# Kernel tuning notes

Measured on AMD Instinct MI355X. Metric: run time of the kernel, lower is better.

## Reference

```python
import jax, jax.numpy as jnp
import numpy as np

N, H, W = 4096, 96, 96
C0 = 0.28209479177387814
C1 = 0.4886025119029199
C2 = [1.0925484305920792, -1.0925484305920792, 0.31539156525252005, -1.0925484305920792, 0.5462742152960396]
C3 = [-0.5900435899266435, 2.890611442640554, -0.4570457994644658, 0.3731763325901154, -0.4570457994644658, 1.445305721320277, -0.5900435899266435]


def setup_inputs() -> dict:
    key = jax.random.key(0)
    ks = jax.random.split(key, 6)
    return {
        'pws': jax.random.normal(ks[0], (N, 3), jnp.float32),
        'low_shs': 0.5 * jax.random.normal(ks[1], (N, 3), jnp.float32),
        'high_shs': 0.1 * jax.random.normal(ks[2], (N, 45), jnp.float32),
        'alphas_raw': jax.random.normal(ks[3], (N, 1), jnp.float32),
        'scales_raw': 0.5 * jax.random.normal(ks[4], (N, 3), jnp.float32) - 3.0,
        'rots_raw': jax.random.normal(ks[5], (N, 4), jnp.float32),
        'us': jnp.zeros((N, 2), jnp.float32),
        'Rcw': jnp.eye(3, dtype=jnp.float32),
        'tcw': jnp.array([0.0, 0.0, 4.0], jnp.float32),
        'cam_intr': jnp.array([120.0, 120.0, 48.0, 48.0], jnp.float32),  # fx fy cx cy
    }


def quat_to_rot(q):
    w, x, y, z = q[:, 0], q[:, 1], q[:, 2], q[:, 3]
    return jnp.stack([
        jnp.stack([1 - 2 * (y * y + z * z), 2 * (x * y - w * z), 2 * (x * z + w * y)], -1),
        jnp.stack([2 * (x * y + w * z), 1 - 2 * (x * x + z * z), 2 * (y * z - w * x)], -1),
        jnp.stack([2 * (x * z - w * y), 2 * (y * z + w * x), 1 - 2 * (x * x + y * y)], -1),
    ], -2)  # [N,3,3]


def sh2color(shs, dirs):
    # shs [N,16,3], dirs [N,3] normalized view directions
    x, y, z = dirs[:, 0:1], dirs[:, 1:2], dirs[:, 2:3]
    xx, yy, zz = x * x, y * y, z * z
    xy, yz, xz = x * y, y * z, x * z
    c = C0 * shs[:, 0]
    c = c - C1 * y * shs[:, 1] + C1 * z * shs[:, 2] - C1 * x * shs[:, 3]
    c = (c + C2[0] * xy * shs[:, 4] + C2[1] * yz * shs[:, 5]
         + C2[2] * (2 * zz - xx - yy) * shs[:, 6]
         + C2[3] * xz * shs[:, 7] + C2[4] * (xx - yy) * shs[:, 8])
    c = (c + C3[0] * y * (3 * xx - yy) * shs[:, 9] + C3[1] * xy * z * shs[:, 10]
         + C3[2] * y * (4 * zz - xx - yy) * shs[:, 11]
         + C3[3] * z * (2 * zz - 3 * xx - 3 * yy) * shs[:, 12]
         + C3[4] * x * (4 * zz - xx - yy) * shs[:, 13]
         + C3[5] * z * (xx - yy) * shs[:, 14]
         + C3[6] * x * (xx - 3 * yy) * shs[:, 15])
    return jnp.maximum(c + 0.5, 0.0)  # [N,3]


def _forward(pws, low_shs, high_shs, alphas_raw, scales_raw, rots_raw, Rcw, tcw, cam_intr):
    fx, fy, cx, cy = cam_intr[0], cam_intr[1], cam_intr[2], cam_intr[3]
    alphas = jax.nn.sigmoid(alphas_raw)[:, 0]                 # get_alphas
    scales = jnp.exp(scales_raw)                              # get_scales
    rots = rots_raw / jnp.linalg.norm(rots_raw, axis=1, keepdims=True)  # get_rots
    shs = jnp.concatenate([low_shs, high_shs], axis=1).reshape(-1, 16, 3)

    # --- project ---
    pcs = pws @ Rcw.T + tcw                                   # [N,3] camera coords
    depths = pcs[:, 2]
    zs = jnp.where(depths > 1e-6, depths, 1e-6)
    u = jnp.stack([fx * pcs[:, 0] / zs + cx, fy * pcs[:, 1] / zs + cy], axis=1)

    # --- cov3d = (R S)(R S)^T ---
    M = quat_to_rot(rots) * scales[:, None, :]
    cov3d = M @ jnp.swapaxes(M, 1, 2)                          # [N,3,3]

    # --- cov2d = J W cov3d W^T J^T + 0.3 I ---
    limx, limy = 1.3 * (W / (2.0 * fx)), 1.3 * (H / (2.0 * fy))
    tx = jnp.clip(pcs[:, 0] / zs, -limx, limx) * zs
    ty = jnp.clip(pcs[:, 1] / zs, -limy, limy) * zs
    zero = jnp.zeros_like(zs)
    J = jnp.stack([
        jnp.stack([fx / zs, zero, -fx * tx / (zs * zs)], -1),
        jnp.stack([zero, fy / zs, -fy * ty / (zs * zs)], -1),
    ], -2)                                                     # [N,2,3]
    T = J @ Rcw
    cov2d = T @ cov3d @ jnp.swapaxes(T, 1, 2)
    a = cov2d[:, 0, 0] + 0.3
    b = cov2d[:, 0, 1]
    c2 = cov2d[:, 1, 1] + 0.3

    # --- inverseCov2D + areas (radius of 3-sigma ellipse) ---
    det = a * c2 - b * b
    cinv = jnp.stack([c2, -b, a], axis=1) / det[:, None]       # [N,3]
    mid = 0.5 * (a + c2)
    lam = mid + jnp.sqrt(jnp.maximum(mid * mid - det, 0.1))
    radius = jnp.ceil(3.0 * jnp.sqrt(lam))
    areas = jnp.stack([radius, radius], axis=1)                # [N,2]

    # --- sh2Color ---
    twc = -(Rcw.T @ tcw)
    dirs = pws - twc
    dirs = dirs / jnp.linalg.norm(dirs, axis=1, keepdims=True)
    colors = sh2color(shs, dirs)                               # [N,3]

    # --- splat: depth-sorted alpha compositing ---
    valid = depths > 0.2
    order = jnp.argsort(depths)
    u_s, cinv_s = u[order], cinv[order]
    alpha_s, color_s, valid_s = alphas[order], colors[order], valid[order]

    px = (jnp.arange(W, dtype=jnp.float32))[None, :].repeat(H, 0).reshape(-1)
    py = (jnp.arange(H, dtype=jnp.float32))[:, None].repeat(W, 1).reshape(-1)
    dx = u_s[:, 0:1] - px[None, :]                             # [N,P]
    dy = u_s[:, 1:2] - py[None, :]
    power = -0.5 * (cinv_s[:, 0:1] * dx * dx + cinv_s[:, 2:3] * dy * dy) - cinv_s[:, 1:2] * dx * dy
    ap = jnp.minimum(alpha_s[:, None] * jnp.exp(jnp.minimum(power, 0.0)), 0.99)
    ap = jnp.where((ap >= 1.0 / 255.0) & valid_s[:, None], ap, 0.0)
    logt = jnp.cumsum(jnp.log1p(-ap), axis=0)
    tau = jnp.exp(jnp.concatenate([jnp.zeros((1, ap.shape[1])), logt[:-1]], axis=0))
    wgt = jnp.where(tau > 1e-4, ap * tau, 0.0)                 # [N,P]
    image = jnp.einsum('nc,np->cp', color_s, wgt).reshape(3, H, W)
    return image, areas


def reference(pws, low_shs, high_shs, alphas_raw, scales_raw, rots_raw, us, Rcw, tcw, cam_intr):
    return _forward(pws, low_shs, high_shs, alphas_raw, scales_raw, rots_raw, Rcw, tcw, cam_intr)
```

## Files before the change

kernel.cpp:

```cpp
#include <hip/hip_runtime.h>
#include <hip/hip_bf16.h>
#include <math.h>

#define GS_N 4096
#define IMG_H 96
#define IMG_W 96
#define NPIX (IMG_H * IMG_W)
#define TILE_PX 12
#define TILES_X 8
#define NTILES (TILES_X * TILES_X)
#define WAVES_PER_TILE 36

#define SH_C0 0.28209479177387814f
#define SH_C1 0.4886025119029199f
__device__ __constant__ float kC2[5] = {1.0925484305920792f, -1.0925484305920792f, 0.31539156525252005f, -1.0925484305920792f, 0.5462742152960396f};
__device__ __constant__ float kC3[7] = {-0.5900435899266435f, 2.890611442640554f, -0.4570457994644658f, 0.3731763325901154f, -0.4570457994644658f, 1.445305721320277f, -0.5900435899266435f};

__global__ __launch_bounds__(256) void gs_prep(
    const float* __restrict__ pws, const float* __restrict__ low_shs,
    const float* __restrict__ high_shs, const float* __restrict__ alphas_raw,
    const float* __restrict__ scales_raw, const float* __restrict__ rots_raw,
    const float* __restrict__ Rcw, const float* __restrict__ tcw,
    const float* __restrict__ cam,
    float* __restrict__ areas_out,
    float* __restrict__ depth_ws,
    int*   __restrict__ rank_ws,
    float4* __restrict__ A_uns,
    float4* __restrict__ B_uns,
    float* __restrict__ C_uns,
    float4* __restrict__ D_uns)
{
    int i = blockIdx.x * 256 + threadIdx.x;
    if (i >= GS_N) return;

    rank_ws[i] = 0;

    float fx = cam[0], fy = cam[1], cxi = cam[2], cyi = cam[3];
    float R0 = Rcw[0], R1 = Rcw[1], R2 = Rcw[2];
    float R3 = Rcw[3], R4 = Rcw[4], R5 = Rcw[5];
    float R6 = Rcw[6], R7 = Rcw[7], R8 = Rcw[8];
    float t0 = tcw[0], t1 = tcw[1], t2 = tcw[2];

    float pwx = pws[3*i+0], pwy = pws[3*i+1], pwz = pws[3*i+2];

    float pcx = R0*pwx + R1*pwy + R2*pwz + t0;
    float pcy = R3*pwx + R4*pwy + R5*pwz + t1;
    float pcz = R6*pwx + R7*pwy + R8*pwz + t2;

    float depth = pcz;
    float zs = (depth > 1e-6f) ? depth : 1e-6f;

    float ux = fx * pcx / zs + cxi;
    float uy = fy * pcy / zs + cyi;

    float alpha = 1.0f / (1.0f + expf(-alphas_raw[i]));

    float s0 = expf(scales_raw[3*i+0]);
    float s1 = expf(scales_raw[3*i+1]);
    float s2 = expf(scales_raw[3*i+2]);

    float qw = rots_raw[4*i+0], qx = rots_raw[4*i+1], qy = rots_raw[4*i+2], qz = rots_raw[4*i+3];
    float qn = sqrtf(qw*qw + qx*qx + qy*qy + qz*qz);
    qw /= qn; qx /= qn; qy /= qn; qz /= qn;

    float r00 = 1.0f - 2.0f*(qy*qy + qz*qz);
    float r01 = 2.0f*(qx*qy - qw*qz);
    float r02 = 2.0f*(qx*qz + qw*qy);
    float r10 = 2.0f*(qx*qy + qw*qz);
    float r11 = 1.0f - 2.0f*(qx*qx + qz*qz);
    float r12 = 2.0f*(qy*qz - qw*qx);
    float r20 = 2.0f*(qx*qz - qw*qy);
    float r21 = 2.0f*(qy*qz + qw*qx);
    float r22 = 1.0f - 2.0f*(qx*qx + qy*qy);

    float m00 = r00*s0, m01 = r01*s1, m02 = r02*s2;
    float m10 = r10*s0, m11 = r11*s1, m12 = r12*s2;
    float m20 = r20*s0, m21 = r21*s1, m22 = r22*s2;

    float V00 = m00*m00 + m01*m01 + m02*m02;
    float V01 = m00*m10 + m01*m11 + m02*m12;
    float V02 = m00*m20 + m01*m21 + m02*m22;
    float V11 = m10*m10 + m11*m11 + m12*m12;
    float V12 = m10*m20 + m11*m21 + m12*m22;
    float V22 = m20*m20 + m21*m21 + m22*m22;

    float limx = 1.3f * ((float)IMG_W / (2.0f * fx));
    float limy = 1.3f * ((float)IMG_H / (2.0f * fy));
    float xzr = pcx / zs, yzr = pcy / zs;
    float txv = fminf(fmaxf(xzr, -limx), limx) * zs;
    float tyv = fminf(fmaxf(yzr, -limy), limy) * zs;

    float J00 = fx / zs, J02 = -fx * txv / (zs * zs);
    float J11 = fy / zs, J12 = -fy * tyv / (zs * zs);

    float T00 = J00*R0 + J02*R6, T01 = J00*R1 + J02*R7, T02 = J00*R2 + J02*R8;
    float T10 = J11*R3 + J12*R6, T11 = J11*R4 + J12*R7, T12 = J11*R5 + J12*R8;

    float TW00 = T00*V00 + T01*V01 + T02*V02;
    float TW01 = T00*V01 + T01*V11 + T02*V12;
    float TW02 = T00*V02 + T01*V12 + T02*V22;
    float TW10 = T10*V00 + T11*V01 + T12*V02;
    float TW11 = T10*V01 + T11*V11 + T12*V12;
    float TW12 = T10*V02 + T11*V12 + T12*V22;

    float c00 = TW00*T00 + TW01*T01 + TW02*T02;
    float c01 = TW00*T10 + TW01*T11 + TW02*T12;
    float c11 = TW10*T10 + TW11*T11 + TW12*T12;

    float a  = c00 + 0.3f;
    float b  = c01;
    float cc = c11 + 0.3f;
    float det = a * cc - b * b;
    float ci0 = cc / det;
    float ci1 = -b / det;
    float ci2 = a / det;

    float mid = 0.5f * (a + cc);
    float lam = mid + sqrtf(fmaxf(mid * mid - det, 0.1f));
    float radius = ceilf(3.0f * sqrtf(lam));
    areas_out[2*i + 0] = radius;
    areas_out[2*i + 1] = radius;

    float twcx = -(R0*t0 + R3*t1 + R6*t2);
    float twcy = -(R1*t0 + R4*t1 + R7*t2);
    float twcz = -(R2*t0 + R5*t1 + R8*t2);
    float dx = pwx - twcx, dy = pwy - twcy, dz = pwz - twcz;
    float dn = sqrtf(dx*dx + dy*dy + dz*dz);
    dx /= dn; dy /= dn; dz /= dn;

    float xx = dx*dx, yy = dy*dy, zz = dz*dz;
    float xy = dx*dy, yz = dy*dz, xz = dx*dz;

    float bas0  = SH_C0;
    float bas1  = -SH_C1 * dy;
    float bas2  =  SH_C1 * dz;
    float bas3  = -SH_C1 * dx;
    float bas4  = kC2[0] * xy;
    float bas5  = kC2[1] * yz;
    float bas6  = kC2[2] * (2.0f*zz - xx - yy);
    float bas7  = kC2[3] * xz;
    float bas8  = kC2[4] * (xx - yy);
    float bas9  = kC3[0] * dy * (3.0f*xx - yy);
    float bas10 = kC3[1] * xy * dz;
    float bas11 = kC3[2] * dy * (4.0f*zz - xx - yy);
    float bas12 = kC3[3] * dz * (2.0f*zz - 3.0f*xx - 3.0f*yy);
    float bas13 = kC3[4] * dx * (4.0f*zz - xx - yy);
    float bas14 = kC3[5] * dz * (xx - yy);
    float bas15 = kC3[6] * dx * (xx - 3.0f*yy);

    float col[3];
    #pragma unroll
    for (int c = 0; c < 3; ++c) {
        const float* hs = high_shs + 45*i + c;
        float acc = bas0 * low_shs[3*i + c];
        acc += bas1  * hs[0*3];
        acc += bas2  * hs[1*3];
        acc += bas3  * hs[2*3];
        acc += bas4  * hs[3*3];
        acc += bas5  * hs[4*3];
        acc += bas6  * hs[5*3];
        acc += bas7  * hs[6*3];
        acc += bas8  * hs[7*3];
        acc += bas9  * hs[8*3];
        acc += bas10 * hs[9*3];
        acc += bas11 * hs[10*3];
        acc += bas12 * hs[11*3];
        acc += bas13 * hs[12*3];
        acc += bas14 * hs[13*3];
        acc += bas15 * hs[14*3];
        col[c] = fmaxf(acc + 0.5f, 0.0f);
    }

    bool valid = depth > 0.2f;
    float al_eff = valid ? alpha : 0.0f;

    float Tthr = __logf(255.0f * al_eff) + 1e-4f;
    float rx = (Tthr > 0.0f) ? sqrtf(2.0f * Tthr * a)  : -1.0f;
    float ry = (Tthr > 0.0f) ? sqrtf(2.0f * Tthr * cc) : -1.0f;

    depth_ws[i] = depth;
    A_uns[i] = make_float4(ux, uy, ci0, ci1);
    B_uns[i] = make_float4(ci2, al_eff, col[0], col[1]);
    C_uns[i] = col[2];
    D_uns[i] = make_float4(ux, uy, rx, ry);
}

__global__ __launch_bounds__(256) void gs_rank_partial(
    const float* __restrict__ depth, int* __restrict__ rank_ws)
{
    __shared__ float sd[256];
    int itile = blockIdx.x >> 4;
    int jtile = blockIdx.x & 15;
    int tid = threadIdx.x;
    int i = itile * 256 + tid;

    sd[tid] = depth[jtile * 256 + tid];
    __syncthreads();

    float mg = depth[i];
    int jbase = jtile * 256;
    int rank = 0;
    const float4* s4 = (const float4*)sd;
    #pragma unroll 16
    for (int jj = 0; jj < 64; ++jj) {
        float4 v = s4[jj];
        int j0 = jbase + jj * 4;
        rank += (v.x < mg || (v.x == mg && (j0+0) < i)) ? 1 : 0;
        rank += (v.y < mg || (v.y == mg && (j0+1) < i)) ? 1 : 0;
        rank += (v.z < mg || (v.z == mg && (j0+2) < i)) ? 1 : 0;
        rank += (v.w < mg || (v.w == mg && (j0+3) < i)) ? 1 : 0;
    }
    atomicAdd(&rank_ws[i], rank);
}

__global__ __launch_bounds__(256) void gs_gather(
    const int* __restrict__ rank_ws,
    const float4* __restrict__ A_uns, const float4* __restrict__ B_uns,
    const float* __restrict__ C_uns, const float4* __restrict__ D_uns,
    float4* __restrict__ A_s, float4* __restrict__ B_s, float* __restrict__ C_s,
    float4* __restrict__ D_s)
{
    int i = blockIdx.x * 256 + threadIdx.x;
    int r = rank_ws[i];
    A_s[r] = A_uns[i];
    B_s[r] = B_uns[i];
    C_s[r] = C_uns[i];
    D_s[r] = D_uns[i];
}

__global__ __launch_bounds__(256) void gs_bin(
    const float4* __restrict__ D_s,
    int* __restrict__ tile_list, int* __restrict__ tile_cnt)
{
    __shared__ int s_base;
    __shared__ int warp_off[4];
    int tile = blockIdx.x;
    int tx = tile & (TILES_X - 1), ty = tile >> 3;
    float x0 = (float)(tx * TILE_PX), x1 = (float)(tx * TILE_PX + TILE_PX - 1);
    float y0 = (float)(ty * TILE_PX), y1 = (float)(ty * TILE_PX + TILE_PX - 1);

    int tid = threadIdx.x;
    int lane = tid & 63, w = tid >> 6;
    if (tid == 0) s_base = 0;
    __syncthreads();

    int* list = tile_list + tile * GS_N;

    for (int r = 0; r < GS_N / 256; ++r) {
        int g = r * 256 + tid;
        float4 d = D_s[g];
        bool pred = (d.z >= 0.0f) &&
                    (d.x - d.z <= x1) && (d.x + d.z >= x0) &&
                    (d.y - d.w <= y1) && (d.y + d.w >= y0);
        unsigned long long m = __ballot(pred);
        int before = __popcll(m & ((1ull << lane) - 1ull));
        int wcnt = __popcll(m);
        if (lane == 0) warp_off[w] = wcnt;
        __syncthreads();
        int off = s_base;
        #pragma unroll
        for (int k = 0; k < 4; ++k) if (k < w) off += warp_off[k];
        if (pred) list[off + before] = g;
        __syncthreads();
        if (tid == 0) s_base += warp_off[0] + warp_off[1] + warp_off[2] + warp_off[3];
    }
    __syncthreads();
    if (tid == 0) tile_cnt[tile] = s_base;
}

__global__ __launch_bounds__(256) void gs_raster(
    const float4* __restrict__ A_s, const float4* __restrict__ B_s,
    const float* __restrict__ C_s,
    const int* __restrict__ tile_list, const int* __restrict__ tile_cnt,
    float* __restrict__ img)
{
    int b = blockIdx.x;
    int tile = b / WAVES_PER_TILE;
    int sub  = b - tile * WAVES_PER_TILE;
    int lane = threadIdx.x & 63;
    int wv   = threadIdx.x >> 6;

    int idxp = sub * 4 + wv;
    int lx = idxp % TILE_PX, ly = idxp / TILE_PX;
    int tx = tile & (TILES_X - 1), ty = tile >> 3;
    int pxi = tx * TILE_PX + lx, pyi = ty * TILE_PX + ly;
    float px = (float)pxi, py = (float)pyi;
    int p = pyi * IMG_W + pxi;

    int cnt = tile_cnt[tile];
    const int* list = tile_list + tile * GS_N;

    float carry = 1.0f;
    float accr = 0.0f, accg = 0.0f, accb = 0.0f;

    for (int c0 = 0; c0 < cnt; c0 += 64) {
        int k = c0 + lane;
        float ap = 0.0f, colr = 0.0f, colg = 0.0f, colb = 0.0f;
        if (k < cnt) {
            int n = list[k];
            float4 a4 = A_s[n];
            float4 b4 = B_s[n];
            colb = C_s[n];
            colr = b4.z; colg = b4.w;

            float ddx = a4.x - px;
            float ddy = a4.y - py;
            float pw = -0.5f * (a4.z * ddx * ddx + b4.x * ddy * ddy) - a4.w * ddx * ddy;
            pw = fminf(pw, 0.0f);
            ap = b4.y * __expf(pw);
            ap = fminf(ap, 0.99f);
            ap = (ap >= (1.0f / 255.0f)) ? ap : 0.0f;
        }

        float f = 1.0f - ap;
        float incl = f;
        #pragma unroll
        for (int d = 1; d < 64; d <<= 1) {
            float v = __shfl_up(incl, d, 64);
            if (lane >= d) incl *= v;
        }
        float excl = __shfl_up(incl, 1, 64);
        if (lane == 0) excl = 1.0f;

        float tau = carry * excl;
        float wgt = (tau > 1e-4f) ? ap * tau : 0.0f;
        accr += colr * wgt;
        accg += colg * wgt;
        accb += colb * wgt;

        carry *= __shfl(incl, 63, 64);
        if (carry <= 1e-4f) break;
    }

    #pragma unroll
    for (int d = 32; d >= 1; d >>= 1) {
        accr += __shfl_xor(accr, d, 64);
        accg += __shfl_xor(accg, d, 64);
        accb += __shfl_xor(accb, d, 64);
    }
    if (lane == 0) {
        img[0 * NPIX + p] = accr;
        img[1 * NPIX + p] = accg;
        img[2 * NPIX + p] = accb;
    }
}

extern "C" void kernel_launch(void* const* d_in, const int* in_sizes, int n_in,
                              void* d_out, int out_size, void* d_ws, size_t ws_size,
                              hipStream_t stream) {
    const float* pws        = (const float*)d_in[0];
    const float* low_shs    = (const float*)d_in[1];
    const float* high_shs   = (const float*)d_in[2];
    const float* alphas_raw = (const float*)d_in[3];
    const float* scales_raw = (const float*)d_in[4];
    const float* rots_raw   = (const float*)d_in[5];
    const float* Rcw        = (const float*)d_in[7];
    const float* tcw        = (const float*)d_in[8];
    const float* cam        = (const float*)d_in[9];

    float* out_img   = (float*)d_out;
    float* out_areas = (float*)d_out + 3 * NPIX;

    char* ws = (char*)d_ws;
    float*  depth_ws = (float*) (ws + 0);
    int*    rank_ws  = (int*)   (ws + 16384);
    float4* A_uns    = (float4*)(ws + 32768);
    float4* B_uns    = (float4*)(ws + 98304);
    float*  C_uns    = (float*) (ws + 163840);
    float4* D_uns    = (float4*)(ws + 180224);
    float4* A_s      = (float4*)(ws + 245760);
    float4* B_s      = (float4*)(ws + 311296);
    float*  C_s      = (float*) (ws + 376832);
    float4* D_s      = (float4*)(ws + 393216);
    int*    tile_cnt = (int*)   (ws + 458752);
    int*    tile_list= (int*)   (ws + 460800);

    gs_prep<<<GS_N / 256, 256, 0, stream>>>(
        pws, low_shs, high_shs, alphas_raw, scales_raw, rots_raw, Rcw, tcw, cam,
        out_areas, depth_ws, rank_ws, A_uns, B_uns, C_uns, D_uns);

    gs_rank_partial<<<256, 256, 0, stream>>>(depth_ws, rank_ws);

    gs_gather<<<GS_N / 256, 256, 0, stream>>>(
        rank_ws, A_uns, B_uns, C_uns, D_uns, A_s, B_s, C_s, D_s);

    gs_bin<<<NTILES, 256, 0, stream>>>(D_s, tile_list, tile_cnt);

    gs_raster<<<NTILES * WAVES_PER_TILE, 256, 0, stream>>>(
        A_s, B_s, C_s, tile_list, tile_cnt, out_img);
}
```

Measured before the change: 101.6 us.

## Fuse gather, binning and rasterization into one per-tile kernel with LDS staging

After: 151.3 us. 49.0% more time.

```diff
diff --git a/kernel.cpp b/kernel.cpp
--- a/kernel.cpp
+++ b/kernel.cpp
@@ -6,10 +6,10 @@
 #define IMG_H 96
 #define IMG_W 96
 #define NPIX (IMG_H * IMG_W)
-#define TILE_PX 12
-#define TILES_X 8
+#define TILE_PX 16
+#define TILES_X 6
 #define NTILES (TILES_X * TILES_X)
-#define WAVES_PER_TILE 36
+#define CHUNK 256
 
 #define SH_C0 0.28209479177387814f
 #define SH_C1 0.4886025119029199f
@@ -213,42 +213,34 @@
     atomicAdd(&rank_ws[i], rank);
 }
 
-__global__ __launch_bounds__(256) void gs_gather(
+__global__ __launch_bounds__(256) void gs_tile(
     const int* __restrict__ rank_ws,
     const float4* __restrict__ A_uns, const float4* __restrict__ B_uns,
     const float* __restrict__ C_uns, const float4* __restrict__ D_uns,
-    float4* __restrict__ A_s, float4* __restrict__ B_s, float* __restrict__ C_s,
-    float4* __restrict__ D_s)
+    float* __restrict__ img)
 {
-    int i = blockIdx.x * 256 + threadIdx.x;
-    int r = rank_ws[i];
-    A_s[r] = A_uns[i];
-    B_s[r] = B_uns[i];
-    C_s[r] = C_uns[i];
-    D_s[r] = D_uns[i];
-}
-
-__global__ __launch_bounds__(256) void gs_bin(
-    const float4* __restrict__ D_s,
-    int* __restrict__ tile_list, int* __restrict__ tile_cnt)
-{
-    __shared__ int s_base;
+    __shared__ int order_lds[GS_N];
+    __shared__ int list[GS_N];
+    __shared__ float4 sA[CHUNK];
+    __shared__ float4 sB[CHUNK];
+    __shared__ float  sC[CHUNK];
     __shared__ int warp_off[4];
+
+    int tid = threadIdx.x;
     int tile = blockIdx.x;
-    int tx = tile & (TILES_X - 1), ty = tile >> 3;
+    int tx = tile % TILES_X, ty = tile / TILES_X;
+
+    #pragma unroll
+    for (int i = tid; i < GS_N; i += 256) order_lds[rank_ws[i]] = i;
+    __syncthreads();
+
     float x0 = (float)(tx * TILE_PX), x1 = (float)(tx * TILE_PX + TILE_PX - 1);
     float y0 = (float)(ty * TILE_PX), y1 = (float)(ty * TILE_PX + TILE_PX - 1);
-
-    int tid = threadIdx.x;
     int lane = tid & 63, w = tid >> 6;
-    if (tid == 0) s_base = 0;
-    __syncthreads();
-
-    int* list = tile_list + tile * GS_N;
-
-    for (int r = 0; r < GS_N / 256; ++r) {
-        int g = r * 256 + tid;
-        float4 d = D_s[g];
+    int base = 0;
+    for (int r0 = 0; r0 < GS_N; r0 += 256) {
+        int i = order_lds[r0 + tid];
+        float4 d = D_uns[i];
         bool pred = (d.z >= 0.0f) &&
                     (d.x - d.z <= x1) && (d.x + d.z >= x0) &&
                     (d.y - d.w <= y1) && (d.y + d.w >= y0);
@@ -257,92 +249,58 @@
         int wcnt = __popcll(m);
         if (lane == 0) warp_off[w] = wcnt;
         __syncthreads();
-        int off = s_base;
-        #pragma unroll
-        for (int k = 0; k < 4; ++k) if (k < w) off += warp_off[k];
-        if (pred) list[off + before] = g;
+        int o0 = warp_off[0], o1 = warp_off[1], o2 = warp_off[2], o3 = warp_off[3];
+        int off = base + ((w > 0) ? o0 : 0) + ((w > 1) ? o1 : 0) + ((w > 2) ? o2 : 0);
+        if (pred) list[off + before] = i;
+        base += o0 + o1 + o2 + o3;
         __syncthreads();
-        if (tid == 0) s_base += warp_off[0] + warp_off[1] + warp_off[2] + warp_off[3];
     }
-    __syncthreads();
-    if (tid == 0) tile_cnt[tile] = s_base;
-}
-
-__global__ __launch_bounds__(256) void gs_raster(
-    const float4* __restrict__ A_s, const float4* __restrict__ B_s,
-    const float* __restrict__ C_s,
-    const int* __restrict__ tile_list, const int* __restrict__ tile_cnt,
-    float* __restrict__ img)
-{
-    int b = blockIdx.x;
-    int tile = b / WAVES_PER_TILE;
-    int sub  = b - tile * WAVES_PER_TILE;
-    int lane = threadIdx.x & 63;
-    int wv   = threadIdx.x >> 6;
-
-    int idxp = sub * 4 + wv;
-    int lx = idxp % TILE_PX, ly = idxp / TILE_PX;
-    int tx = tile & (TILES_X - 1), ty = tile >> 3;
+    int cnt = base;
+
+    int lx = tid & (TILE_PX - 1), ly = tid >> 4;
     int pxi = tx * TILE_PX + lx, pyi = ty * TILE_PX + ly;
     float px = (float)pxi, py = (float)pyi;
     int p = pyi * IMG_W + pxi;
 
-    int cnt = tile_cnt[tile];
-    const int* list = tile_list + tile * GS_N;
-
-    float carry = 1.0f;
+    float tau = 1.0f;
     float accr = 0.0f, accg = 0.0f, accb = 0.0f;
-
-    for (int c0 = 0; c0 < cnt; c0 += 64) {
-        int k = c0 + lane;
-        float ap = 0.0f, colr = 0.0f, colg = 0.0f, colb = 0.0f;
+    bool done = false;
+
+    for (int c0 = 0; c0 < cnt; c0 += CHUNK) {
+        int k = c0 + tid;
         if (k < cnt) {
             int n = list[k];
-            float4 a4 = A_s[n];
-            float4 b4 = B_s[n];
-            colb = C_s[n];
-            colr = b4.z; colg = b4.w;
-
-            float ddx = a4.x - px;
-            float ddy = a4.y - py;
-            float pw = -0.5f * (a4.z * ddx * ddx + b4.x * ddy * ddy) - a4.w * ddx * ddy;
-            pw = fminf(pw, 0.0f);
-            ap = b4.y * __expf(pw);
-            ap = fminf(ap, 0.99f);
-            ap = (ap >= (1.0f / 255.0f)) ? ap : 0.0f;
+            sA[tid] = A_uns[n];
+            sB[tid] = B_uns[n];
+            sC[tid] = C_uns[n];
         }
-
-        float f = 1.0f - ap;
-        float incl = f;
-        #pragma unroll
-        for (int d = 1; d < 64; d <<= 1) {
-            float v = __shfl_up(incl, d, 64);
-            if (lane >= d) incl *= v;
+        __syncthreads();
+        int mm = min(CHUNK, cnt - c0);
+        if (!done) {
+            for (int j = 0; j < mm; ++j) {
+                float4 a4 = sA[j];
+                float4 b4 = sB[j];
+                float ddx = a4.x - px;
+                float ddy = a4.y - py;
+                float pw = -0.5f * (a4.z * ddx * ddx + b4.x * ddy * ddy) - a4.w * ddx * ddy;
+                pw = fminf(pw, 0.0f);
+                float ap = b4.y * __expf(pw);
+                ap = fminf(ap, 0.99f);
+                ap = (ap >= (1.0f / 255.0f)) ? ap : 0.0f;
+                float wgt = ap * tau;
+                accr += b4.z * wgt;
+                accg += b4.w * wgt;
+                accb += sC[j] * wgt;
+                tau *= 1.0f - ap;
+                if (tau <= 1e-4f) { done = true; break; }
+            }
         }
-        float excl = __shfl_up(incl, 1, 64);
-        if (lane == 0) excl = 1.0f;
-
-        float tau = carry * excl;
-        float wgt = (tau > 1e-4f) ? ap * tau : 0.0f;
-        accr += colr * wgt;
-        accg += colg * wgt;
-        accb += colb * wgt;
-
-        carry *= __shfl(incl, 63, 64);
-        if (carry <= 1e-4f) break;
+        if (__syncthreads_and((int)done)) break;
     }
 
-    #pragma unroll
-    for (int d = 32; d >= 1; d >>= 1) {
-        accr += __shfl_xor(accr, d, 64);
-        accg += __shfl_xor(accg, d, 64);
-        accb += __shfl_xor(accb, d, 64);
-    }
-    if (lane == 0) {
-        img[0 * NPIX + p] = accr;
-        img[1 * NPIX + p] = accg;
-        img[2 * NPIX + p] = accb;
-    }
+    img[0 * NPIX + p] = accr;
+    img[1 * NPIX + p] = accg;
+    img[2 * NPIX + p] = accb;
 }
 
 extern "C" void kernel_launch(void* const* d_in, const int* in_sizes, int n_in,
@@ -368,12 +326,6 @@
     float4* B_uns    = (float4*)(ws + 98304);
     float*  C_uns    = (float*) (ws + 163840);
     float4* D_uns    = (float4*)(ws + 180224);
-    float4* A_s      = (float4*)(ws + 245760);
-    float4* B_s      = (float4*)(ws + 311296);
-    float*  C_s      = (float*) (ws + 376832);
-    float4* D_s      = (float4*)(ws + 393216);
-    int*    tile_cnt = (int*)   (ws + 458752);
-    int*    tile_list= (int*)   (ws + 460800);
 
     gs_prep<<<GS_N / 256, 256, 0, stream>>>(
         pws, low_shs, high_shs, alphas_raw, scales_raw, rots_raw, Rcw, tcw, cam,
@@ -381,11 +333,6 @@
 
     gs_rank_partial<<<256, 256, 0, stream>>>(depth_ws, rank_ws);
 
-    gs_gather<<<GS_N / 256, 256, 0, stream>>>(
-        rank_ws, A_uns, B_uns, C_uns, D_uns, A_s, B_s, C_s, D_s);
-
-    gs_bin<<<NTILES, 256, 0, stream>>>(D_s, tile_list, tile_cnt);
-
-    gs_raster<<<NTILES * WAVES_PER_TILE, 256, 0, stream>>>(
-        A_s, B_s, C_s, tile_list, tile_cnt, out_img);
+    gs_tile<<<NTILES, 256, 0, stream>>>(
+        rank_ws, A_uns, B_uns, C_uns, D_uns, out_img);
 }
```

## Fold gather into binning via LDS inverse permutation and skip empty raster chunks

Applied to the files above, without the earlier changes.

Result: no change. 101.8 us (+0.2%).

```diff
diff --git a/kernel.cpp b/kernel.cpp
--- a/kernel.cpp
+++ b/kernel.cpp
@@ -213,26 +213,12 @@
     atomicAdd(&rank_ws[i], rank);
 }
 
-__global__ __launch_bounds__(256) void gs_gather(
+__global__ __launch_bounds__(256) void gs_bin2(
     const int* __restrict__ rank_ws,
-    const float4* __restrict__ A_uns, const float4* __restrict__ B_uns,
-    const float* __restrict__ C_uns, const float4* __restrict__ D_uns,
-    float4* __restrict__ A_s, float4* __restrict__ B_s, float* __restrict__ C_s,
-    float4* __restrict__ D_s)
-{
-    int i = blockIdx.x * 256 + threadIdx.x;
-    int r = rank_ws[i];
-    A_s[r] = A_uns[i];
-    B_s[r] = B_uns[i];
-    C_s[r] = C_uns[i];
-    D_s[r] = D_uns[i];
-}
-
-__global__ __launch_bounds__(256) void gs_bin(
-    const float4* __restrict__ D_s,
+    const float4* __restrict__ D_uns,
     int* __restrict__ tile_list, int* __restrict__ tile_cnt)
 {
-    __shared__ int s_base;
+    __shared__ int order_lds[GS_N];
     __shared__ int warp_off[4];
     int tile = blockIdx.x;
     int tx = tile & (TILES_X - 1), ty = tile >> 3;
@@ -241,14 +227,17 @@
 
     int tid = threadIdx.x;
     int lane = tid & 63, w = tid >> 6;
-    if (tid == 0) s_base = 0;
+
+    #pragma unroll
+    for (int i = tid; i < GS_N; i += 256) order_lds[rank_ws[i]] = i;
     __syncthreads();
 
     int* list = tile_list + tile * GS_N;
-
-    for (int r = 0; r < GS_N / 256; ++r) {
-        int g = r * 256 + tid;
-        float4 d = D_s[g];
+    int base = 0;
+
+    for (int r0 = 0; r0 < GS_N; r0 += 256) {
+        int i = order_lds[r0 + tid];
+        float4 d = D_uns[i];
         bool pred = (d.z >= 0.0f) &&
                     (d.x - d.z <= x1) && (d.x + d.z >= x0) &&
                     (d.y - d.w <= y1) && (d.y + d.w >= y0);
@@ -257,20 +246,18 @@
         int wcnt = __popcll(m);
         if (lane == 0) warp_off[w] = wcnt;
         __syncthreads();
-        int off = s_base;
-        #pragma unroll
-        for (int k = 0; k < 4; ++k) if (k < w) off += warp_off[k];
-        if (pred) list[off + before] = g;
+        int o0 = warp_off[0], o1 = warp_off[1], o2 = warp_off[2], o3 = warp_off[3];
+        int off = base + ((w > 0) ? o0 : 0) + ((w > 1) ? o1 : 0) + ((w > 2) ? o2 : 0);
+        if (pred) list[off + before] = i;
+        base += o0 + o1 + o2 + o3;
         __syncthreads();
-        if (tid == 0) s_base += warp_off[0] + warp_off[1] + warp_off[2] + warp_off[3];
-    }
-    __syncthreads();
-    if (tid == 0) tile_cnt[tile] = s_base;
+    }
+    if (tid == 0) tile_cnt[tile] = base;
 }
 
 __global__ __launch_bounds__(256) void gs_raster(
-    const float4* __restrict__ A_s, const float4* __restrict__ B_s,
-    const float* __restrict__ C_s,
+    const float4* __restrict__ A_uns, const float4* __restrict__ B_uns,
+    const float* __restrict__ C_uns,
     const int* __restrict__ tile_list, const int* __restrict__ tile_cnt,
     float* __restrict__ img)
 {
@@ -298,9 +285,9 @@
         float ap = 0.0f, colr = 0.0f, colg = 0.0f, colb = 0.0f;
         if (k < cnt) {
             int n = list[k];
-            float4 a4 = A_s[n];
-            float4 b4 = B_s[n];
-            colb = C_s[n];
+            float4 a4 = A_uns[n];
+            float4 b4 = B_uns[n];
+            colb = C_uns[n];
             colr = b4.z; colg = b4.w;
 
             float ddx = a4.x - px;
@@ -311,6 +298,8 @@
             ap = fminf(ap, 0.99f);
             ap = (ap >= (1.0f / 255.0f)) ? ap : 0.0f;
         }
+
+        if (__ballot(ap > 0.0f) == 0ull) continue;
 
         float f = 1.0f - ap;
         float incl = f;
@@ -368,12 +357,8 @@
     float4* B_uns    = (float4*)(ws + 98304);
     float*  C_uns    = (float*) (ws + 163840);
     float4* D_uns    = (float4*)(ws + 180224);
-    float4* A_s      = (float4*)(ws + 245760);
-    float4* B_s      = (float4*)(ws + 311296);
-    float*  C_s      = (float*) (ws + 376832);
-    float4* D_s      = (float4*)(ws + 393216);
-    int*    tile_cnt = (int*)   (ws + 458752);
-    int*    tile_list= (int*)   (ws + 460800);
+    int*    tile_cnt = (int*)   (ws + 245760);
+    int*    tile_list= (int*)   (ws + 247808);
 
     gs_prep<<<GS_N / 256, 256, 0, stream>>>(
         pws, low_shs, high_shs, alphas_raw, scales_raw, rots_raw, Rcw, tcw, cam,
@@ -381,11 +366,8 @@
 
     gs_rank_partial<<<256, 256, 0, stream>>>(depth_ws, rank_ws);
 
-    gs_gather<<<GS_N / 256, 256, 0, stream>>>(
-        rank_ws, A_uns, B_uns, C_uns, D_uns, A_s, B_s, C_s, D_s);
-
-    gs_bin<<<NTILES, 256, 0, stream>>>(D_s, tile_list, tile_cnt);
+    gs_bin2<<<NTILES, 256, 0, stream>>>(rank_ws, D_uns, tile_list, tile_cnt);
 
     gs_raster<<<NTILES * WAVES_PER_TILE, 256, 0, stream>>>(
-        A_s, B_s, C_s, tile_list, tile_cnt, out_img);
-}
+        A_uns, B_uns, C_uns, tile_list, tile_cnt, out_img);
+}
```

## Replace per-tile binning kernel with atomic bitmask tiles built during gather

Applied to the files above, without the earlier changes.

Measured after the change: 96.26 us. -5.2%, faster.

```diff
diff --git a/kernel.cpp b/kernel.cpp
--- a/kernel.cpp
+++ b/kernel.cpp
@@ -28,12 +28,14 @@
     float4* __restrict__ A_uns,
     float4* __restrict__ B_uns,
     float* __restrict__ C_uns,
-    float4* __restrict__ D_uns)
+    float4* __restrict__ D_uns,
+    unsigned long long* __restrict__ mask_ws)
 {
     int i = blockIdx.x * 256 + threadIdx.x;
     if (i >= GS_N) return;
 
     rank_ws[i] = 0;
+    mask_ws[i] = 0ull;
 
     float fx = cam[0], fy = cam[1], cxi = cam[2], cyi = cam[3];
     float R0 = Rcw[0], R1 = Rcw[1], R2 = Rcw[2];
@@ -213,72 +215,69 @@
     atomicAdd(&rank_ws[i], rank);
 }
 
-__global__ __launch_bounds__(256) void gs_gather(
+__global__ __launch_bounds__(256) void gs_gather_mask(
     const int* __restrict__ rank_ws,
     const float4* __restrict__ A_uns, const float4* __restrict__ B_uns,
     const float* __restrict__ C_uns, const float4* __restrict__ D_uns,
     float4* __restrict__ A_s, float4* __restrict__ B_s, float* __restrict__ C_s,
-    float4* __restrict__ D_s)
+    unsigned long long* __restrict__ mask_ws)
 {
     int i = blockIdx.x * 256 + threadIdx.x;
     int r = rank_ws[i];
     A_s[r] = A_uns[i];
     B_s[r] = B_uns[i];
     C_s[r] = C_uns[i];
-    D_s[r] = D_uns[i];
-}
-
-__global__ __launch_bounds__(256) void gs_bin(
-    const float4* __restrict__ D_s,
-    int* __restrict__ tile_list, int* __restrict__ tile_cnt)
-{
-    __shared__ int s_base;
-    __shared__ int warp_off[4];
-    int tile = blockIdx.x;
-    int tx = tile & (TILES_X - 1), ty = tile >> 3;
-    float x0 = (float)(tx * TILE_PX), x1 = (float)(tx * TILE_PX + TILE_PX - 1);
-    float y0 = (float)(ty * TILE_PX), y1 = (float)(ty * TILE_PX + TILE_PX - 1);
-
-    int tid = threadIdx.x;
-    int lane = tid & 63, w = tid >> 6;
-    if (tid == 0) s_base = 0;
-    __syncthreads();
-
-    int* list = tile_list + tile * GS_N;
-
-    for (int r = 0; r < GS_N / 256; ++r) {
-        int g = r * 256 + tid;
-        float4 d = D_s[g];
-        bool pred = (d.z >= 0.0f) &&
-                    (d.x - d.z <= x1) && (d.x + d.z >= x0) &&
-                    (d.y - d.w <= y1) && (d.y + d.w >= y0);
-        unsigned long long m = __ballot(pred);
-        int before = __popcll(m & ((1ull << lane) - 1ull));
-        int wcnt = __popcll(m);
-        if (lane == 0) warp_off[w] = wcnt;
-        __syncthreads();
-        int off = s_base;
-        #pragma unroll
-        for (int k = 0; k < 4; ++k) if (k < w) off += warp_off[k];
-        if (pred) list[off + before] = g;
-        __syncthreads();
-        if (tid == 0) s_base += warp_off[0] + warp_off[1] + warp_off[2] + warp_off[3];
-    }
-    __syncthreads();
-    if (tid == 0) tile_cnt[tile] = s_base;
+
+    float4 d = D_uns[i];
+    if (d.z >= 0.0f) {
+        const float inv = 1.0f / (float)TILE_PX;
+        int tx0 = max(0, (int)ceilf((d.x - d.z - (float)(TILE_PX - 1)) * inv - 1e-4f));
+        int tx1 = min(TILES_X - 1, (int)floorf((d.x + d.z) * inv + 1e-4f));
+        int ty0 = max(0, (int)ceilf((d.y - d.w - (float)(TILE_PX - 1)) * inv - 1e-4f));
+        int ty1 = min(TILES_X - 1, (int)floorf((d.y + d.w) * inv + 1e-4f));
+        unsigned long long bit = 1ull << (r & 63);
+        int w = r >> 6;
+        for (int ty = ty0; ty <= ty1; ++ty)
+            for (int tx = tx0; tx <= tx1; ++tx)
+                atomicOr(&mask_ws[(ty * TILES_X + tx) * 64 + w], bit);
+    }
 }
 
 __global__ __launch_bounds__(256) void gs_raster(
     const float4* __restrict__ A_s, const float4* __restrict__ B_s,
     const float* __restrict__ C_s,
-    const int* __restrict__ tile_list, const int* __restrict__ tile_cnt,
+    const unsigned long long* __restrict__ mask_ws,
     float* __restrict__ img)
 {
+    __shared__ unsigned short slist[GS_N];
+    __shared__ int scnt;
+
     int b = blockIdx.x;
     int tile = b / WAVES_PER_TILE;
     int sub  = b - tile * WAVES_PER_TILE;
     int lane = threadIdx.x & 63;
     int wv   = threadIdx.x >> 6;
+
+    if (wv == 0) {
+        unsigned long long m = mask_ws[tile * 64 + lane];
+        int c = __popcll(m);
+        int incl = c;
+        #pragma unroll
+        for (int d = 1; d < 64; d <<= 1) {
+            int v = __shfl_up(incl, d, 64);
+            if (lane >= d) incl += v;
+        }
+        int off = incl - c;
+        int base = lane << 6;
+        while (m) {
+            int bpos = __builtin_ctzll(m);
+            m &= m - 1;
+            slist[off++] = (unsigned short)(base + bpos);
+        }
+        if (lane == 63) scnt = incl;
+    }
+    __syncthreads();
+    int cnt = scnt;
 
     int idxp = sub * 4 + wv;
     int lx = idxp % TILE_PX, ly = idxp / TILE_PX;
@@ -287,9 +286,6 @@
     float px = (float)pxi, py = (float)pyi;
     int p = pyi * IMG_W + pxi;
 
-    int cnt = tile_cnt[tile];
-    const int* list = tile_list + tile * GS_N;
-
     float carry = 1.0f;
     float accr = 0.0f, accg = 0.0f, accb = 0.0f;
 
@@ -297,7 +293,7 @@
         int k = c0 + lane;
         float ap = 0.0f, colr = 0.0f, colg = 0.0f, colb = 0.0f;
         if (k < cnt) {
-            int n = list[k];
+            int n = slist[k];
             float4 a4 = A_s[n];
             float4 b4 = B_s[n];
             colb = C_s[n];
@@ -311,6 +307,8 @@
             ap = fminf(ap, 0.99f);
             ap = (ap >= (1.0f / 255.0f)) ? ap : 0.0f;
         }
+
+        if (__ballot(ap > 0.0f) == 0ull) continue;
 
         float f = 1.0f - ap;
         float incl = f;
@@ -371,21 +369,17 @@
     float4* A_s      = (float4*)(ws + 245760);
     float4* B_s      = (float4*)(ws + 311296);
     float*  C_s      = (float*) (ws + 376832);
-    float4* D_s      = (float4*)(ws + 393216);
-    int*    tile_cnt = (int*)   (ws + 458752);
-    int*    tile_list= (int*)   (ws + 460800);
+    unsigned long long* mask_ws = (unsigned long long*)(ws + 393216);
 
     gs_prep<<<GS_N / 256, 256, 0, stream>>>(
         pws, low_shs, high_shs, alphas_raw, scales_raw, rots_raw, Rcw, tcw, cam,
-        out_areas, depth_ws, rank_ws, A_uns, B_uns, C_uns, D_uns);
+        out_areas, depth_ws, rank_ws, A_uns, B_uns, C_uns, D_uns, mask_ws);
 
     gs_rank_partial<<<256, 256, 0, stream>>>(depth_ws, rank_ws);
 
-    gs_gather<<<GS_N / 256, 256, 0, stream>>>(
-        rank_ws, A_uns, B_uns, C_uns, D_uns, A_s, B_s, C_s, D_s);
-
-    gs_bin<<<NTILES, 256, 0, stream>>>(D_s, tile_list, tile_cnt);
+    gs_gather_mask<<<GS_N / 256, 256, 0, stream>>>(
+        rank_ws, A_uns, B_uns, C_uns, D_uns, A_s, B_s, C_s, mask_ws);
 
     gs_raster<<<NTILES * WAVES_PER_TILE, 256, 0, stream>>>(
-        A_s, B_s, C_s, tile_list, tile_cnt, out_img);
-}
+        A_s, B_s, C_s, mask_ws, out_img);
+}
```
